# Kernel tuning notes

Measured on AMD Instinct MI355X. Metric: run time of the kernel, lower is better.

## Reference

```python
import jax, jax.numpy as jnp
import numpy as np


def setup_inputs() -> dict:
    key = jax.random.key(0)
    k1, k2 = jax.random.split(key)
    B, C, H, W, D = 2, 1, 128, 128, 128
    image = jax.random.normal(k1, (B, C, H, W, D), dtype=jnp.float32)
    # dense displacement field in voxel units (typical registration magnitudes)
    ddf = jax.random.normal(k2, (B, 3, H, W, D), dtype=jnp.float32) * 3.0
    return {"image": image, "ddf": ddf}


def _warp(image, ddf):
    """Trilinear grid_sample warp, padding_mode='zeros', align_corners=True.

    Equivalent to MONAI Warp(mode=1, padding_mode='zeros'): the reference grid
    plus DDF gives absolute voxel coordinates; torch's normalization to [-1,1]
    with align_corners=True followed by grid_sample maps exactly back to these
    voxel coordinates, so we sample directly in voxel space.
    """
    B, C, H, W, D = image.shape
    dt = image.dtype
    mesh = jnp.stack(
        jnp.meshgrid(
            jnp.arange(H, dtype=dt),
            jnp.arange(W, dtype=dt),
            jnp.arange(D, dtype=dt),
            indexing="ij",
        ),
        axis=-1,
    )  # (H, W, D, 3)
    coords = mesh[None] + jnp.moveaxis(ddf, 1, -1)  # (B, H, W, D, 3) voxel coords

    c0f = jnp.floor(coords)
    frac = coords - c0f                      # (B, H, W, D, 3)
    c0 = c0f.astype(jnp.int32)
    sizes = jnp.array([H, W, D], dtype=jnp.int32)
    strides = jnp.array([W * D, D, 1], dtype=jnp.int32)

    N = H * W * D
    img_flat = image.reshape(B, C, N)
    out = jnp.zeros((B, C, N), dtype=dt)
    # 8 trilinear taps; zeros padding => out-of-range taps contribute 0
    for dx in (0, 1):
        for dy in (0, 1):
            for dz in (0, 1):
                off = jnp.array([dx, dy, dz], dtype=jnp.int32)
                idx = c0 + off                                   # (B,H,W,D,3)
                wsel = jnp.where(off == 1, frac, 1.0 - frac)
                w = wsel[..., 0] * wsel[..., 1] * wsel[..., 2]   # (B,H,W,D)
                valid = jnp.all((idx >= 0) & (idx < sizes), axis=-1)
                idxc = jnp.clip(idx, 0, sizes - 1)
                lin = jnp.sum(idxc * strides, axis=-1).reshape(B, N)
                vals = jax.vmap(lambda im, li: im[:, li])(img_flat, lin)  # (B,C,N)
                out = out + vals * (w * valid.astype(dt)).reshape(B, 1, N)
    return out.reshape(B, C, H, W, D)


def reference(image, ddf):
    return _warp(image, ddf)
```

## Files before the change

### kernel.cpp

```cpp
#include <hip/hip_runtime.h>
#include <hip/hip_fp16.h>


constexpr int H = 128, W = 128, D = 128;
constexpr int N = H * W * D;
constexpr int B = 2;
constexpr int HA = 8;
constexpr int RS = 32;
constexpr int RN = RS * RS * RS;

typedef float fvec4 __attribute__((ext_vector_type(4)));
typedef unsigned u2v __attribute__((ext_vector_type(2), aligned(4)));

__global__ __launch_bounds__(1024, 8) void warp_tile_kernel(
    const float* __restrict__ image,
    const float* __restrict__ ddf,
    float* __restrict__ out)
{
    __shared__ __half tile[RN];

    int bid = blockIdx.x;
    int T   = (bid & 7) * 128 + (bid >> 3);
    int b  = T >> 9;
    int t3 = T & 511;
    int tx0 = ((t3 >> 6) & 7) << 4;
    int ty0 = ((t3 >> 3) & 7) << 4;
    int tz0 = (t3 & 7) << 4;
    int ox = tx0 - HA, oy = ty0 - HA, oz = tz0 - HA;

    const float* img = image + ((size_t)b << 21);
    int t = threadIdx.x;

    int zq = (t & 3) << 2;
    int ly = (t >> 2) & 15;
    int lx = t >> 6;
    int vx = tx0 + lx, vy = ty0 + ly, vz = tz0 + zq;
    int lin0 = (vx << 14) + (vy << 7) + vz;

    const float* ddfb = ddf + (size_t)b * 3 * N;
    fvec4 dx4 = *(const fvec4*)(ddfb + lin0);
    fvec4 dy4 = *(const fvec4*)(ddfb + lin0 + N);
    fvec4 dz4 = *(const fvec4*)(ddfb + lin0 + 2 * N);

    fvec4 sa[4], sb[4];
    int rows[4], zos[4];
#pragma unroll
    for (int c = 0; c < 4; ++c) {
        int s   = c * 1024 + t;
        int row = s >> 2;
        int zo  = (s & 3) << 3;
        rows[c] = row; zos[c] = zo;
        int gx = ox + (row >> 5);
        int gy = oy + (row & 31);
        int gz = oz + zo;
        bool ok = ((unsigned)gx < 128u) & ((unsigned)gy < 128u) & ((unsigned)gz < 121u);
        const float* p = img + (gx << 14) + (gy << 7) + gz;
        fvec4 z4 = {0.f, 0.f, 0.f, 0.f};
        sa[c] = ok ? *(const fvec4*)p       : z4;
        sb[c] = ok ? *(const fvec4*)(p + 4) : z4;
    }
    unsigned short* tp = (unsigned short*)tile;
#pragma unroll
    for (int c = 0; c < 4; ++c) {
        __half2 h0 = __floats2half2_rn(sa[c].x, sa[c].y);
        __half2 h1 = __floats2half2_rn(sa[c].z, sa[c].w);
        __half2 h2 = __floats2half2_rn(sb[c].x, sb[c].y);
        __half2 h3 = __floats2half2_rn(sb[c].z, sb[c].w);
        uint4 pk;
        pk.x = *(unsigned int*)&h0;
        pk.y = *(unsigned int*)&h1;
        pk.z = *(unsigned int*)&h2;
        pk.w = *(unsigned int*)&h3;
        *(uint4*)(tp + rows[c] * 32 + zos[c]) = pk;
    }
    __syncthreads();

    float* outb = out + ((size_t)b << 21);
    const unsigned int* cells = (const unsigned int*)tile;
    float dxp[4] = {dx4.x, dx4.y, dx4.z, dx4.w};
    float dyp[4] = {dy4.x, dy4.y, dy4.z, dy4.w};
    float dzp[4] = {dz4.x, dz4.y, dz4.z, dz4.w};
    float res[4];

#pragma unroll
    for (int i = 0; i < 4; ++i) {
        float x = (float)vx + dxp[i];
        float y = (float)vy + dyp[i];
        float z = (float)(vz + i) + dzp[i];

        float xf = floorf(x), yf = floorf(y), zf = floorf(z);
        float fx = x - xf, fy = y - yf, fz = z - zf;
        int x0 = (int)xf, y0 = (int)yf, z0 = (int)zf;
        int rx = x0 - ox, ry = y0 - oy, rz = z0 - oz;

        float acc;
        if ((unsigned)rx <= 30u && (unsigned)ry <= 30u && (unsigned)rz <= 30u) {
            int rowc = ((rx << 5) + ry) << 4;
            int c  = rowc + (rz >> 1);
            int sh = (rz & 1) << 4;
            u2v q00 = *(const u2v*)(cells + c);
            u2v q01 = *(const u2v*)(cells + c + 16);
            u2v q10 = *(const u2v*)(cells + c + 512);
            u2v q11 = *(const u2v*)(cells + c + 528);

            float az0 = 1.f - fz;
            float zz[4];
            unsigned los[4] = {q00.x, q01.x, q10.x, q11.x};
            unsigned his[4] = {q00.y, q01.y, q10.y, q11.y};
#pragma unroll
            for (int p2 = 0; p2 < 4; ++p2) {
                unsigned long long v = ((unsigned long long)his[p2] << 32) | los[p2];
                unsigned pr = (unsigned)(v >> sh);
                __half2 hp = *(__half2*)&pr;
                float2 f2 = __half22float2(hp);
                zz[p2] = az0 * f2.x + fz * f2.y;
            }
            float ay0 = 1.f - fy;
            acc = (1.f - fx) * (ay0 * zz[0] + fy * zz[1]) +
                  fx         * (ay0 * zz[2] + fy * zz[3]);
        } else {
            int x1 = x0 + 1, y1 = y0 + 1, z1 = z0 + 1;
            bool vx0 = (unsigned)x0 < (unsigned)H;
            bool vx1 = (unsigned)x1 < (unsigned)H;
            bool vy0 = (unsigned)y0 < (unsigned)W;
            bool vy1 = (unsigned)y1 < (unsigned)W;
            bool vz0 = (unsigned)z0 < (unsigned)D;
            bool vz1 = (unsigned)z1 < (unsigned)D;
            float ax0 = vx0 ? (1.0f - fx) : 0.0f;
            float ax1 = vx1 ? fx          : 0.0f;
            float ay0 = vy0 ? (1.0f - fy) : 0.0f;
            float ay1 = vy1 ? fy          : 0.0f;
            float az0 = vz0 ? (1.0f - fz) : 0.0f;
            float az1 = vz1 ? fz          : 0.0f;
            int cx0 = vx0 ? x0 : 0;
            int cx1 = vx1 ? x1 : 0;
            int cy0 = vy0 ? y0 : 0;
            int cy1 = vy1 ? y1 : 0;
            int cz0 = vz0 ? z0 : 0;
            int cz1 = vz1 ? z1 : 0;
            int rx0 = cx0 << 14, rx1 = cx1 << 14;
            int ry0 = cy0 << 7,  ry1 = cy1 << 7;
            float v000 = img[rx0 + ry0 + cz0];
            float v001 = img[rx0 + ry0 + cz1];
            float v010 = img[rx0 + ry1 + cz0];
            float v011 = img[rx0 + ry1 + cz1];
            float v100 = img[rx1 + ry0 + cz0];
            float v101 = img[rx1 + ry0 + cz1];
            float v110 = img[rx1 + ry1 + cz0];
            float v111 = img[rx1 + ry1 + cz1];
            acc = ax0 * (ay0 * (az0 * v000 + az1 * v001) +
                         ay1 * (az0 * v010 + az1 * v011)) +
                  ax1 * (ay0 * (az0 * v100 + az1 * v101) +
                         ay1 * (az0 * v110 + az1 * v111));
        }
        res[i] = acc;
    }
    fvec4 r4 = {res[0], res[1], res[2], res[3]};
    __builtin_nontemporal_store(r4, (fvec4*)(outb + lin0));
}

extern "C" void kernel_launch(void* const* d_in, const int* in_sizes, int n_in,
                              void* d_out, int out_size, void* d_ws, size_t ws_size,
                              hipStream_t stream) {
    const float* image = (const float*)d_in[0];
    const float* ddf   = (const float*)d_in[1];
    float* out = (float*)d_out;

    warp_tile_kernel<<<B * 512, 1024, 0, stream>>>(image, ddf, out);
}
```

Baseline: 104.2 us.

## Replace fp16 shared-memory halo tile with direct global trilinear gathers

Removes the per-block staging of a 32^3 halo region into LDS as fp16, along with the barrier, and has every output voxel gather its 8 taps straight from global memory through the cache. This drops the cooperative tile load (which reads roughly 8x the block's own voxel count), the fp16 conversion and the sync, and it restores full fp32 precision. In exchange, every tap now becomes a scattered global load that depends on cache locality, where before most taps were LDS hits.

```diff
diff --git a/kernel.cpp b/kernel.cpp
--- a/kernel.cpp
+++ b/kernel.cpp
@@ -1,24 +1,17 @@
 #include <hip/hip_runtime.h>
-#include <hip/hip_fp16.h>
 
 
 constexpr int H = 128, W = 128, D = 128;
 constexpr int N = H * W * D;
 constexpr int B = 2;
-constexpr int HA = 8;
-constexpr int RS = 32;
-constexpr int RN = RS * RS * RS;
 
 typedef float fvec4 __attribute__((ext_vector_type(4)));
-typedef unsigned u2v __attribute__((ext_vector_type(2), aligned(4)));
 
-__global__ __launch_bounds__(1024, 8) void warp_tile_kernel(
+__global__ __launch_bounds__(1024, 8) void warp_gather_kernel(
     const float* __restrict__ image,
     const float* __restrict__ ddf,
     float* __restrict__ out)
 {
-    __shared__ __half tile[RN];
-
     int bid = blockIdx.x;
     int T   = (bid & 7) * 128 + (bid >> 3);
     int b  = T >> 9;
@@ -26,7 +19,6 @@
     int tx0 = ((t3 >> 6) & 7) << 4;
     int ty0 = ((t3 >> 3) & 7) << 4;
     int tz0 = (t3 & 7) << 4;
-    int ox = tx0 - HA, oy = ty0 - HA, oz = tz0 - HA;
 
     const float* img = image + ((size_t)b << 21);
     int t = threadIdx.x;
@@ -42,41 +34,6 @@
     fvec4 dy4 = *(const fvec4*)(ddfb + lin0 + N);
     fvec4 dz4 = *(const fvec4*)(ddfb + lin0 + 2 * N);
 
-    fvec4 sa[4], sb[4];
-    int rows[4], zos[4];
-#pragma unroll
-    for (int c = 0; c < 4; ++c) {
-        int s   = c * 1024 + t;
-        int row = s >> 2;
-        int zo  = (s & 3) << 3;
-        rows[c] = row; zos[c] = zo;
-        int gx = ox + (row >> 5);
-        int gy = oy + (row & 31);
-        int gz = oz + zo;
-        bool ok = ((unsigned)gx < 128u) & ((unsigned)gy < 128u) & ((unsigned)gz < 121u);
-        const float* p = img + (gx << 14) + (gy << 7) + gz;
-        fvec4 z4 = {0.f, 0.f, 0.f, 0.f};
-        sa[c] = ok ? *(const fvec4*)p       : z4;
-        sb[c] = ok ? *(const fvec4*)(p + 4) : z4;
-    }
-    unsigned short* tp = (unsigned short*)tile;
-#pragma unroll
-    for (int c = 0; c < 4; ++c) {
-        __half2 h0 = __floats2half2_rn(sa[c].x, sa[c].y);
-        __half2 h1 = __floats2half2_rn(sa[c].z, sa[c].w);
-        __half2 h2 = __floats2half2_rn(sb[c].x, sb[c].y);
-        __half2 h3 = __floats2half2_rn(sb[c].z, sb[c].w);
-        uint4 pk;
-        pk.x = *(unsigned int*)&h0;
-        pk.y = *(unsigned int*)&h1;
-        pk.z = *(unsigned int*)&h2;
-        pk.w = *(unsigned int*)&h3;
-        *(uint4*)(tp + rows[c] * 32 + zos[c]) = pk;
-    }
-    __syncthreads();
-
-    float* outb = out + ((size_t)b << 21);
-    const unsigned int* cells = (const unsigned int*)tile;
     float dxp[4] = {dx4.x, dx4.y, dx4.z, dx4.w};
     float dyp[4] = {dy4.x, dy4.y, dy4.z, dy4.w};
     float dzp[4] = {dz4.x, dz4.y, dz4.z, dz4.w};
@@ -91,70 +48,48 @@
         float xf = floorf(x), yf = floorf(y), zf = floorf(z);
         float fx = x - xf, fy = y - yf, fz = z - zf;
         int x0 = (int)xf, y0 = (int)yf, z0 = (int)zf;
-        int rx = x0 - ox, ry = y0 - oy, rz = z0 - oz;
+        int x1 = x0 + 1, y1 = y0 + 1, z1 = z0 + 1;
 
-        float acc;
-        if ((unsigned)rx <= 30u && (unsigned)ry <= 30u && (unsigned)rz <= 30u) {
-            int rowc = ((rx << 5) + ry) << 4;
-            int c  = rowc + (rz >> 1);
-            int sh = (rz & 1) << 4;
-            u2v q00 = *(const u2v*)(cells + c);
-            u2v q01 = *(const u2v*)(cells + c + 16);
-            u2v q10 = *(const u2v*)(cells + c + 512);
-            u2v q11 = *(const u2v*)(cells + c + 528);
+        bool bx0 = (unsigned)x0 < (unsigned)H;
+        bool bx1 = (unsigned)x1 < (unsigned)H;
+        bool by0 = (unsigned)y0 < (unsigned)W;
+        bool by1 = (unsigned)y1 < (unsigned)W;
+        bool bz0 = (unsigned)z0 < (unsigned)D;
+        bool bz1 = (unsigned)z1 < (unsigned)D;
+        float ax0 = bx0 ? (1.0f - fx) : 0.0f;
+        float ax1 = bx1 ? fx          : 0.0f;
+        float ay0 = by0 ? (1.0f - fy) : 0.0f;
+        float ay1 = by1 ? fy          : 0.0f;
+        float az0 = bz0 ? (1.0f - fz) : 0.0f;
+        float az1 = bz1 ? fz          : 0.0f;
+        int cx0 = bx0 ? x0 : 0;
+        int cx1 = bx1 ? x1 : 0;
+        int cy0 = by0 ? y0 : 0;
+        int cy1 = by1 ? y1 : 0;
+        int cz0 = bz0 ? z0 : 0;
+        int cz1 = bz1 ? z1 : 0;
 
-            float az0 = 1.f - fz;
-            float zz[4];
-            unsigned los[4] = {q00.x, q01.x, q10.x, q11.x};
-            unsigned his[4] = {q00.y, q01.y, q10.y, q11.y};
-#pragma unroll
-            for (int p2 = 0; p2 < 4; ++p2) {
-                unsigned long long v = ((unsigned long long)his[p2] << 32) | los[p2];
-                unsigned pr = (unsigned)(v >> sh);
-                __half2 hp = *(__half2*)&pr;
-                float2 f2 = __half22float2(hp);
-                zz[p2] = az0 * f2.x + fz * f2.y;
-            }
-            float ay0 = 1.f - fy;
-            acc = (1.f - fx) * (ay0 * zz[0] + fy * zz[1]) +
-                  fx         * (ay0 * zz[2] + fy * zz[3]);
-        } else {
-            int x1 = x0 + 1, y1 = y0 + 1, z1 = z0 + 1;
-            bool vx0 = (unsigned)x0 < (unsigned)H;
-            bool vx1 = (unsigned)x1 < (unsigned)H;
-            bool vy0 = (unsigned)y0 < (unsigned)W;
-            bool vy1 = (unsigned)y1 < (unsigned)W;
-            bool vz0 = (unsigned)z0 < (unsigned)D;
-            bool vz1 = (unsigned)z1 < (unsigned)D;
-            float ax0 = vx0 ? (1.0f - fx) : 0.0f;
-            float ax1 = vx1 ? fx          : 0.0f;
-            float ay0 = vy0 ? (1.0f - fy) : 0.0f;
-            float ay1 = vy1 ? fy          : 0.0f;
-            float az0 = vz0 ? (1.0f - fz) : 0.0f;
-            float az1 = vz1 ? fz          : 0.0f;
-            int cx0 = vx0 ? x0 : 0;
-            int cx1 = vx1 ? x1 : 0;
-            int cy0 = vy0 ? y0 : 0;
-            int cy1 = vy1 ? y1 : 0;
-            int cz0 = vz0 ? z0 : 0;
-            int cz1 = vz1 ? z1 : 0;
-            int rx0 = cx0 << 14, rx1 = cx1 << 14;
-            int ry0 = cy0 << 7,  ry1 = cy1 << 7;
-            float v000 = img[rx0 + ry0 + cz0];
-            float v001 = img[rx0 + ry0 + cz1];
-            float v010 = img[rx0 + ry1 + cz0];
-            float v011 = img[rx0 + ry1 + cz1];
-            float v100 = img[rx1 + ry0 + cz0];
-            float v101 = img[rx1 + ry0 + cz1];
-            float v110 = img[rx1 + ry1 + cz0];
-            float v111 = img[rx1 + ry1 + cz1];
-            acc = ax0 * (ay0 * (az0 * v000 + az1 * v001) +
-                         ay1 * (az0 * v010 + az1 * v011)) +
-                  ax1 * (ay0 * (az0 * v100 + az1 * v101) +
-                         ay1 * (az0 * v110 + az1 * v111));
-        }
-        res[i] = acc;
+        int rx0 = cx0 << 14, rx1 = cx1 << 14;
+        int ry0 = cy0 << 7,  ry1 = cy1 << 7;
+        int a00 = rx0 + ry0, a01 = rx0 + ry1;
+        int a10 = rx1 + ry0, a11 = rx1 + ry1;
+
+        float v000 = img[a00 + cz0];
+        float v001 = img[a00 + cz1];
+        float v010 = img[a01 + cz0];
+        float v011 = img[a01 + cz1];
+        float v100 = img[a10 + cz0];
+        float v101 = img[a10 + cz1];
+        float v110 = img[a11 + cz0];
+        float v111 = img[a11 + cz1];
+
+        res[i] = ax0 * (ay0 * (az0 * v000 + az1 * v001) +
+                        ay1 * (az0 * v010 + az1 * v011)) +
+                 ax1 * (ay0 * (az0 * v100 + az1 * v101) +
+                        ay1 * (az0 * v110 + az1 * v111));
     }
+
+    float* outb = out + ((size_t)b << 21);
     fvec4 r4 = {res[0], res[1], res[2], res[3]};
     __builtin_nontemporal_store(r4, (fvec4*)(outb + lin0));
 }
@@ -166,5 +101,5 @@
     const float* ddf   = (const float*)d_in[1];
     float* out = (float*)d_out;
 
-    warp_tile_kernel<<<B * 512, 1024, 0, stream>>>(image, ddf, out);
+    warp_gather_kernel<<<B * 512, 1024, 0, stream>>>(image, ddf, out);
 }
```

Result: slower. 154.3 us (+48.0%).
